# Kernel optimization log

Hardware: AMD Instinct MI355X
Metric: run time of the kernel (lower is better)

## Reference

```python
import jax, jax.numpy as jnp
import numpy as np

N_HEAD = 16
MA_K = 0.02          # sigmoid temperature in ma_k_activation
LEAKY_SLOPE = 0.02   # negative_slope in ma_q_activation
NEG_INF = -1e9


def setup_inputs() -> dict:
    key = jax.random.key(0)
    k1, k2, k3, k4 = jax.random.split(key, 4)
    B, T, C = 2, 2048, 1024
    x = jax.random.normal(k1, (B, T, C), dtype=jnp.float32)
    s = 1.0 / np.sqrt(C)
    W_attn = jax.random.normal(k2, (C, 2 * C), dtype=jnp.float32) * s
    W_k2 = jax.random.normal(k3, (C, C), dtype=jnp.float32) * s
    W_proj = jax.random.normal(k4, (C, C), dtype=jnp.float32) * s
    return {"x": x, "W_attn": W_attn, "W_k2": W_k2, "W_proj": W_proj}


def _heads(t, H):
    # [B,T,C] -> [B,H,T,d]
    B, T, C = t.shape
    return t.reshape(B, T, H, C // H).transpose(0, 2, 1, 3)


def reference(x, W_attn, W_k2, W_proj):
    B, T, C = x.shape
    H = N_HEAD
    d = C // H
    scale = 1.0 / jnp.sqrt(jnp.asarray(d, x.dtype))

    qk = x @ W_attn                      # [B,T,2C]
    q, k = jnp.split(qk, 2, axis=-1)
    q = _heads(q, H)                     # [B,H,T,d]
    k = _heads(k, H)
    v = _heads(x, H)                     # v = x

    # --- AR branch: causal softmax attention ---
    scores = jnp.einsum('bhtd,bhsd->bhts', q, k) * scale
    causal = jnp.tril(jnp.ones((T, T), dtype=bool))
    scores = jnp.where(causal, scores, NEG_INF)
    attn = jax.nn.softmax(scores, axis=-1)
    y = jnp.einsum('bhts,bhsd->bhtd', attn, v)   # [B,H,T,d]

    # --- MA branch: causal, softmax-free linear attention on residual ---
    e = v[:, :, 1:, :] - y[:, :, :-1, :]          # [B,H,T-1,d]
    k2 = _heads(x[:, :-1, :] @ W_k2, H)           # [B,H,T-1,d]
    q2 = q[:, :, 1:, :]                           # [B,H,T-1,d]

    qa = -jax.nn.leaky_relu(-q2 * scale, negative_slope=LEAKY_SLOPE)
    ka = jax.nn.sigmoid(MA_K * (k2 * scale))

    w = jnp.einsum('bhtd,bhsd->bhts', qa, ka)     # [B,H,T-1,T-1]
    w = jnp.tril(w)
    y2 = jnp.einsum('bhts,bhsd->bhtd', w, e)      # [B,H,T-1,d]
    y2 = jnp.concatenate([jnp.zeros_like(y2[:, :, :1, :]), y2], axis=2)  # pad front

    def merge(t):  # [B,H,T,d] -> [B,T,C]
        return t.transpose(0, 2, 1, 3).reshape(B, T, C)

    return merge(y) @ W_proj + merge(y2) @ W_proj
```

## Files before the change

kernel.cpp:

```cpp
#include <hip/hip_runtime.h>

typedef unsigned short u16;
typedef u16   u16x4  __attribute__((ext_vector_type(4)));
typedef u16   u16x8  __attribute__((ext_vector_type(8)));
typedef __bf16 bf16x8 __attribute__((ext_vector_type(8)));
typedef float  f32x4  __attribute__((ext_vector_type(4)));

__device__ __forceinline__ float bf2f(u16 v) {
    unsigned u = ((unsigned)v) << 16;
    return __builtin_bit_cast(float, u);
}
__device__ __forceinline__ u16 f2bf(float f) {
    unsigned u = __builtin_bit_cast(unsigned, f);
    u += 0x7fffu + ((u >> 16) & 1u);
    return (u16)(u >> 16);
}

__global__ __launch_bounds__(256)
void convert_f32_bf16(const float* __restrict__ in, u16* __restrict__ out, int n4) {
    int i = blockIdx.x * 256 + threadIdx.x;
    if (i < n4) {
        float4 v = ((const float4*)in)[i];
        u16x4 o;
        o.x = f2bf(v.x); o.y = f2bf(v.y); o.z = f2bf(v.z); o.w = f2bf(v.w);
        ((u16x4*)out)[i] = o;
    }
}

__global__ __launch_bounds__(256)
void transpose_f32_bf16(const float* __restrict__ in, u16* __restrict__ out,
                        int R, int Cd) {
    __shared__ u16 tile[64][65];
    const int c0 = blockIdx.x * 64, r0 = blockIdx.y * 64;
    const int tid = threadIdx.x;
#pragma unroll
    for (int i = 0; i < 16; ++i) {
        int idx = tid + i * 256;
        int r = idx >> 6, c = idx & 63;
        tile[r][c] = f2bf(in[(size_t)(r0 + r) * Cd + c0 + c]);
    }
    __syncthreads();
#pragma unroll
    for (int i = 0; i < 16; ++i) {
        int idx = tid + i * 256;
        int r = idx >> 6, c = idx & 63;
        out[(size_t)(c0 + r) * R + r0 + c] = tile[c][r];
    }
}

template <int EPI>
__global__ __launch_bounds__(256, 2)
void gemm_bt(const u16* __restrict__ A, const u16* __restrict__ Bt,
             void* __restrict__ Cv, int M, int N, int K) {
    __shared__ __align__(16) u16 As[4][128][8];
    __shared__ __align__(16) u16 Bs[4][128][8];
    const int tid = threadIdx.x;
    const int wave = tid >> 6, lane = tid & 63;
    const int m0 = blockIdx.y * 128, n0 = blockIdx.x * 128;
    const int wm = (wave >> 1) * 64, wn = (wave & 1) * 64;
    const int q = lane >> 4, mr = lane & 15;
    const int sr = tid >> 2, c8 = tid & 3;
    const u16* Ap = A + (size_t)(m0 + sr) * K + c8 * 8;
    const u16* Bp = Bt + (size_t)(n0 + sr) * K + c8 * 8;

    f32x4 acc[4][4];
#pragma unroll
    for (int i = 0; i < 4; ++i)
#pragma unroll
        for (int j = 0; j < 4; ++j) acc[i][j] = f32x4{0.f, 0.f, 0.f, 0.f};

    for (int k0 = 0; k0 < K; k0 += 32) {
        u16x8 a0 = *(const u16x8*)(Ap);
        u16x8 a1 = *(const u16x8*)(Ap + (size_t)64 * K);
        u16x8 b0 = *(const u16x8*)(Bp);
        u16x8 b1 = *(const u16x8*)(Bp + (size_t)64 * K);
        Ap += 32; Bp += 32;
        __syncthreads();
        *(u16x8*)&As[c8][sr][0]      = a0;
        *(u16x8*)&As[c8][sr + 64][0] = a1;
        *(u16x8*)&Bs[c8][sr][0]      = b0;
        *(u16x8*)&Bs[c8][sr + 64][0] = b1;
        __syncthreads();
        bf16x8 af[4], bfr[4];
#pragma unroll
        for (int i = 0; i < 4; ++i) af[i]  = *(const bf16x8*)&As[q][wm + i * 16 + mr][0];
#pragma unroll
        for (int j = 0; j < 4; ++j) bfr[j] = *(const bf16x8*)&Bs[q][wn + j * 16 + mr][0];
#pragma unroll
        for (int i = 0; i < 4; ++i)
#pragma unroll
            for (int j = 0; j < 4; ++j)
                acc[i][j] = __builtin_amdgcn_mfma_f32_16x16x32_bf16(af[i], bfr[j], acc[i][j], 0, 0, 0);
    }
    const float qsc = (n0 + wn < 1024) ? 0.125f : 1.0f;
#pragma unroll
    for (int i = 0; i < 4; ++i)
#pragma unroll
        for (int j = 0; j < 4; ++j)
#pragma unroll
            for (int r = 0; r < 4; ++r) {
                int m = m0 + wm + i * 16 + q * 4 + r;
                int n = n0 + wn + j * 16 + mr;
                float v = acc[i][j][r];
                if (EPI == 1)      ((float*)Cv)[(size_t)m * N + n] = v;
                else if (EPI == 2) ((u16*)Cv)[(size_t)m * N + n] = f2bf(1.f / (1.f + __expf(-0.0025f * v)));
                else               ((u16*)Cv)[(size_t)m * N + n] = f2bf(v * qsc);
            }
}

__global__ __launch_bounds__(256, 2)
void flash_mfma(const u16* __restrict__ qk, const u16* __restrict__ xb,
                const float* __restrict__ xf, u16* __restrict__ y,
                u16* __restrict__ eg) {
    __shared__ __align__(16) u16 Ks[8][64][8];
    __shared__ __align__(16) u16 Vs[8][64][8];
    __shared__ __align__(16) u16 Ps[4][16][72];
    const int bh = blockIdx.y, b = bh >> 4, h = bh & 15, hc = h * 64;
    const int tid = threadIdx.x, w = tid >> 6, lane = tid & 63;
    const int n16 = lane & 15, quad = lane >> 4;
    const int sK = tid >> 2, d0 = (tid & 3) * 8;
    const int vcol = lane;

    for (int rep = 0; rep < 2; ++rep) {
        const int tile = rep ? 31 - (int)blockIdx.x : (int)blockIdx.x;
        const int t0 = tile * 64;
        const int nchunk = tile + 1;

        bf16x8 qf[2];
        {
            const int trow = t0 + w * 16 + n16;
            const u16* qp = &qk[(size_t)(b * 2048 + trow) * 2048 + hc + quad * 8];
            qf[0] = *(const bf16x8*)qp;
            qf[1] = *(const bf16x8*)(qp + 32);
        }

        f32x4 O[4];
        float lsum[4];
#pragma unroll
        for (int jt = 0; jt < 4; ++jt) O[jt] = f32x4{0.f, 0.f, 0.f, 0.f};
#pragma unroll
        for (int r = 0; r < 4; ++r) lsum[r] = 0.f;

        u16x8 kr0, kr1;
        u16 vr[16];
        auto prefetch = [&](int s0) {
            size_t krow = (size_t)(b * 2048 + s0 + sK) * 2048 + 1024 + hc;
            kr0 = *(const u16x8*)&qk[krow + d0];
            kr1 = *(const u16x8*)&qk[krow + d0 + 32];
#pragma unroll
            for (int j = 0; j < 8; ++j) {
                vr[j]     = xb[(size_t)(b * 2048 + s0 + w * 8 + j) * 1024 + hc + vcol];
                vr[j + 8] = xb[(size_t)(b * 2048 + s0 + (w + 4) * 8 + j) * 1024 + hc + vcol];
            }
        };
        prefetch(0);

        for (int c = 0; c < nchunk; ++c) {
            const int s0 = c << 6;
            __syncthreads();
            *(u16x8*)&Ks[(d0 >> 3)][sK][0]     = kr0;
            *(u16x8*)&Ks[(d0 >> 3) + 4][sK][0] = kr1;
            {
                u16x8 va, vb;
#pragma unroll
                for (int j = 0; j < 8; ++j) { va[j] = vr[j]; vb[j] = vr[j + 8]; }
                *(u16x8*)&Vs[w][vcol][0]     = va;
                *(u16x8*)&Vs[w + 4][vcol][0] = vb;
            }
            __syncthreads();
            if (c + 1 < nchunk) prefetch(s0 + 64);

            f32x4 S[4];
#pragma unroll
            for (int jt = 0; jt < 4; ++jt) S[jt] = f32x4{0.f, 0.f, 0.f, 0.f};
#pragma unroll
            for (int ks = 0; ks < 2; ++ks)
#pragma unroll
                for (int jt = 0; jt < 4; ++jt) {
                    bf16x8 kf = *(const bf16x8*)&Ks[ks * 4 + quad][jt * 16 + n16][0];
                    S[jt] = __builtin_amdgcn_mfma_f32_16x16x32_bf16(qf[ks], kf, S[jt], 0, 0, 0);
                }

            float p[4][4];
#pragma unroll
            for (int reg = 0; reg < 4; ++reg)
#pragma unroll
                for (int jt = 0; jt < 4; ++jt)
                    p[reg][jt] = __expf(S[jt][reg] - 16.0f);
            if (c == nchunk - 1) {
#pragma unroll
                for (int reg = 0; reg < 4; ++reg) {
                    const int tr = t0 + w * 16 + quad * 4 + reg;
#pragma unroll
                    for (int jt = 0; jt < 4; ++jt)
                        if (s0 + jt * 16 + n16 > tr) p[reg][jt] = 0.f;
                }
            }
#pragma unroll
            for (int reg = 0; reg < 4; ++reg) {
                lsum[reg] += (p[reg][0] + p[reg][1]) + (p[reg][2] + p[reg][3]);
#pragma unroll
                for (int jt = 0; jt < 4; ++jt)
                    Ps[w][quad * 4 + reg][jt * 16 + n16] = f2bf(p[reg][jt]);
            }

            bf16x8 pf[2];
#pragma unroll
            for (int ks = 0; ks < 2; ++ks)
                pf[ks] = *(const bf16x8*)&Ps[w][n16][ks * 32 + quad * 8];
#pragma unroll
            for (int ks = 0; ks < 2; ++ks)
#pragma unroll
                for (int jt = 0; jt < 4; ++jt) {
                    bf16x8 vf = *(const bf16x8*)&Vs[ks * 4 + quad][jt * 16 + n16][0];
                    O[jt] = __builtin_amdgcn_mfma_f32_16x16x32_bf16(pf[ks], vf, O[jt], 0, 0, 0);
                }
        }

#pragma unroll
        for (int reg = 0; reg < 4; ++reg) {
            float l = lsum[reg];
#pragma unroll
            for (int off = 1; off < 16; off <<= 1) l += __shfl_xor(l, off, 64);
            const float inv = 1.f / l;
            const int tr = t0 + w * 16 + quad * 4 + reg;
            const size_t row = (size_t)(b * 2048 + tr) * 1024 + hc;
#pragma unroll
            for (int jt = 0; jt < 4; ++jt) {
                const int col = jt * 16 + n16;
                float yv = O[jt][reg] * inv;
                y[row + col] = f2bf(yv);
                float ev = (tr < 2047) ? xf[row + 1024 + col] - yv : 0.f;
                eg[row + col] = f2bf(ev);
            }
        }
    }
}

__global__ __launch_bounds__(256, 2)
void arma_mfma(const u16* __restrict__ qk, const u16* __restrict__ ka,
               const u16* __restrict__ eg, const u16* __restrict__ y,
               u16* __restrict__ ys) {
    __shared__ __align__(16) u16 Ks[8][64][8];
    __shared__ __align__(16) u16 Es[8][64][8];
    __shared__ __align__(16) u16 Ps[4][16][72];
    const int bh = blockIdx.y, b = bh >> 4, h = bh & 15, hc = h * 64;
    const int tid = threadIdx.x, w = tid >> 6, lane = tid & 63;
    const int n16 = lane & 15, quad = lane >> 4;
    const int sK = tid >> 2, d0 = (tid & 3) * 8;
    const int vcol = lane;

    for (int rep = 0; rep < 2; ++rep) {
        const int tile = rep ? 31 - (int)blockIdx.x : (int)blockIdx.x;
        const int t0 = tile * 64;
        const int nchunk = tile + 1;

        bf16x8 qf[2];
        {
            const int trow = t0 + w * 16 + n16;
            const u16* qp = &qk[(size_t)(b * 2048 + trow) * 2048 + hc + quad * 8];
#pragma unroll
            for (int ks = 0; ks < 2; ++ks) {
                u16x8 qv = *(const u16x8*)(qp + ks * 32);
                u16x8 o;
#pragma unroll
                for (int j = 0; j < 8; ++j) {
                    float z = bf2f(qv[j]);
                    o[j] = f2bf(z < 0.f ? z : 0.02f * z);
                }
                qf[ks] = __builtin_bit_cast(bf16x8, o);
            }
        }

        f32x4 O[4];
#pragma unroll
        for (int jt = 0; jt < 4; ++jt) O[jt] = f32x4{0.f, 0.f, 0.f, 0.f};

        u16x8 kr0, kr1;
        u16 vr[16];
        auto prefetch = [&](int s0) {
            size_t krow = (size_t)(b * 2048 + s0 + sK) * 1024 + hc;
            kr0 = *(const u16x8*)&ka[krow + d0];
            kr1 = *(const u16x8*)&ka[krow + d0 + 32];
#pragma unroll
            for (int j = 0; j < 8; ++j) {
                vr[j]     = eg[(size_t)(b * 2048 + s0 + w * 8 + j) * 1024 + hc + vcol];
                vr[j + 8] = eg[(size_t)(b * 2048 + s0 + (w + 4) * 8 + j) * 1024 + hc + vcol];
            }
        };
        prefetch(0);

        for (int c = 0; c < nchunk; ++c) {
            const int s0 = c << 6;
            __syncthreads();
            *(u16x8*)&Ks[(d0 >> 3)][sK][0]     = kr0;
            *(u16x8*)&Ks[(d0 >> 3) + 4][sK][0] = kr1;
            {
                u16x8 va, vb;
#pragma unroll
                for (int j = 0; j < 8; ++j) { va[j] = vr[j]; vb[j] = vr[j + 8]; }
                *(u16x8*)&Es[w][vcol][0]     = va;
                *(u16x8*)&Es[w + 4][vcol][0] = vb;
            }
            __syncthreads();
            if (c + 1 < nchunk) prefetch(s0 + 64);

            f32x4 S[4];
#pragma unroll
            for (int jt = 0; jt < 4; ++jt) S[jt] = f32x4{0.f, 0.f, 0.f, 0.f};
#pragma unroll
            for (int ks = 0; ks < 2; ++ks)
#pragma unroll
                for (int jt = 0; jt < 4; ++jt) {
                    bf16x8 kf = *(const bf16x8*)&Ks[ks * 4 + quad][jt * 16 + n16][0];
                    S[jt] = __builtin_amdgcn_mfma_f32_16x16x32_bf16(qf[ks], kf, S[jt], 0, 0, 0);
                }

            float p[4][4];
#pragma unroll
            for (int reg = 0; reg < 4; ++reg)
#pragma unroll
                for (int jt = 0; jt < 4; ++jt) p[reg][jt] = S[jt][reg];
            if (c == nchunk - 1) {
#pragma unroll
                for (int reg = 0; reg < 4; ++reg) {
                    const int tr = t0 + w * 16 + quad * 4 + reg;
#pragma unroll
                    for (int jt = 0; jt < 4; ++jt)
                        if (s0 + jt * 16 + n16 >= tr) p[reg][jt] = 0.f;
                }
            }
#pragma unroll
            for (int reg = 0; reg < 4; ++reg)
#pragma unroll
                for (int jt = 0; jt < 4; ++jt)
                    Ps[w][quad * 4 + reg][jt * 16 + n16] = f2bf(p[reg][jt]);

            bf16x8 pf[2];
#pragma unroll
            for (int ks = 0; ks < 2; ++ks)
                pf[ks] = *(const bf16x8*)&Ps[w][n16][ks * 32 + quad * 8];
#pragma unroll
            for (int ks = 0; ks < 2; ++ks)
#pragma unroll
                for (int jt = 0; jt < 4; ++jt) {
                    bf16x8 ef = *(const bf16x8*)&Es[ks * 4 + quad][jt * 16 + n16][0];
                    O[jt] = __builtin_amdgcn_mfma_f32_16x16x32_bf16(pf[ks], ef, O[jt], 0, 0, 0);
                }
        }

#pragma unroll
        for (int reg = 0; reg < 4; ++reg) {
            const int tr = t0 + w * 16 + quad * 4 + reg;
            const size_t row = (size_t)(b * 2048 + tr) * 1024 + hc;
#pragma unroll
            for (int jt = 0; jt < 4; ++jt) {
                const int col = jt * 16 + n16;
                ys[row + col] = f2bf(bf2f(y[row + col]) + O[jt][reg]);
            }
        }
    }
}

extern "C" void kernel_launch(void* const* d_in, const int* in_sizes, int n_in,
                              void* d_out, int out_size, void* d_ws, size_t ws_size,
                              hipStream_t stream) {
    const float* x      = (const float*)d_in[0];
    const float* W_attn = (const float*)d_in[1];
    const float* W_k2   = (const float*)d_in[2];
    const float* W_proj = (const float*)d_in[3];
    float* out = (float*)d_out;

    char* w = (char*)d_ws;
    u16* xb      = (u16*)w; w += (size_t)4096 * 1024 * 2;
    u16* Wt_attn = (u16*)w; w += (size_t)2048 * 1024 * 2;
    u16* Wt_k2   = (u16*)w; w += (size_t)1024 * 1024 * 2;
    u16* Wt_proj = (u16*)w; w += (size_t)1024 * 1024 * 2;
    u16* qk      = (u16*)w; w += (size_t)4096 * 2048 * 2;
    u16* ka      = (u16*)w; w += (size_t)4096 * 1024 * 2;
    u16* y       = (u16*)w; w += (size_t)4096 * 1024 * 2;
    u16* eg      = (u16*)w; w += (size_t)4096 * 1024 * 2;
    u16* ys      = (u16*)w; w += (size_t)4096 * 1024 * 2;

    convert_f32_bf16<<<dim3(4096), dim3(256), 0, stream>>>(x, xb, 1024 * 1024);
    transpose_f32_bf16<<<dim3(32, 16), dim3(256), 0, stream>>>(W_attn, Wt_attn, 1024, 2048);
    transpose_f32_bf16<<<dim3(16, 16), dim3(256), 0, stream>>>(W_k2,   Wt_k2,   1024, 1024);
    transpose_f32_bf16<<<dim3(16, 16), dim3(256), 0, stream>>>(W_proj, Wt_proj, 1024, 1024);
    gemm_bt<3><<<dim3(16, 32), dim3(256), 0, stream>>>(xb, Wt_attn, qk, 4096, 2048, 1024);
    gemm_bt<2><<<dim3(8, 32), dim3(256), 0, stream>>>(xb, Wt_k2, ka, 4096, 1024, 1024);
    flash_mfma<<<dim3(16, 32), dim3(256), 0, stream>>>(qk, xb, x, y, eg);
    arma_mfma<<<dim3(16, 32), dim3(256), 0, stream>>>(qk, ka, eg, y, ys);
    gemm_bt<1><<<dim3(8, 32), dim3(256), 0, stream>>>(ys, Wt_proj, out, 4096, 1024, 1024);
}
```

Baseline: 286.6 us.

## Pre-pack K/V tiles, split attention KV across two partitions, add combine kernels

K, sigmoid-K, V (x) and the residual e are now written by producer kernels in a pre-swizzled per-64-row tile layout, so the attention kernels load LDS tiles with contiguous 16-byte copies instead of strided scalar gathers. Both attention kernels split the key chunks between two z-partitions, raising occupancy (launch bounds 4). Separate combine kernels then sum the partials, normalise, and build y, e and ys. The GEMMs gain register prefetch of the next k-slice, and the N=1024 GEMMs use 64-row tiles for more blocks. This costs extra launches and extra global traffic for the bf16 partial outputs.

```diff
diff --git a/kernel.cpp b/kernel.cpp
--- a/kernel.cpp
+++ b/kernel.cpp
@@ -16,15 +16,29 @@
     return (u16)(u >> 16);
 }
 
+__device__ __forceinline__ size_t kimg_idx(int bh, int s, int d) {
+    return ((size_t)(bh * 32 + (s >> 6)) * 4096) + (size_t)(((d >> 3) * 64 + (s & 63)) * 8) + (d & 7);
+}
+__device__ __forceinline__ size_t vimg_idx(int bh, int s, int d) {
+    return ((size_t)(bh * 32 + (s >> 6)) * 4096) + (size_t)((((s & 63) >> 3) * 64 + d) * 8) + (s & 7);
+}
+
 __global__ __launch_bounds__(256)
-void convert_f32_bf16(const float* __restrict__ in, u16* __restrict__ out, int n4) {
+void convert_pack(const float* __restrict__ in, u16* __restrict__ xb,
+                  u16* __restrict__ xpack) {
     int i = blockIdx.x * 256 + threadIdx.x;
-    if (i < n4) {
-        float4 v = ((const float4*)in)[i];
-        u16x4 o;
-        o.x = f2bf(v.x); o.y = f2bf(v.y); o.z = f2bf(v.z); o.w = f2bf(v.w);
-        ((u16x4*)out)[i] = o;
-    }
+    int c4 = i & 255, row = i >> 8;
+    int s = row & 2047, b = row >> 11;
+    float4 v = ((const float4*)in)[i];
+    u16x4 o;
+    o.x = f2bf(v.x); o.y = f2bf(v.y); o.z = f2bf(v.z); o.w = f2bf(v.w);
+    ((u16x4*)xb)[i] = o;
+    int h = c4 >> 4, d0 = (c4 & 15) * 4;
+    size_t base = vimg_idx(b * 16 + h, s, d0);
+    xpack[base]      = o.x;
+    xpack[base + 8]  = o.y;
+    xpack[base + 16] = o.z;
+    xpack[base + 24] = o.w;
 }
 
 __global__ __launch_bounds__(256)
@@ -48,10 +62,9 @@
     }
 }
 
-template <int EPI>
 __global__ __launch_bounds__(256, 2)
-void gemm_bt(const u16* __restrict__ A, const u16* __restrict__ Bt,
-             void* __restrict__ Cv, int M, int N, int K) {
+void gemm_qk(const u16* __restrict__ A, const u16* __restrict__ Bt,
+             u16* __restrict__ qs, u16* __restrict__ kpack, int K) {
     __shared__ __align__(16) u16 As[4][128][8];
     __shared__ __align__(16) u16 Bs[4][128][8];
     const int tid = threadIdx.x;
@@ -69,18 +82,22 @@
 #pragma unroll
         for (int j = 0; j < 4; ++j) acc[i][j] = f32x4{0.f, 0.f, 0.f, 0.f};
 
+    u16x8 a0, a1, b0, b1;
+    auto gload = [&](int k0) {
+        a0 = *(const u16x8*)(Ap + k0);
+        a1 = *(const u16x8*)(Ap + k0 + (size_t)64 * K);
+        b0 = *(const u16x8*)(Bp + k0);
+        b1 = *(const u16x8*)(Bp + k0 + (size_t)64 * K);
+    };
+    gload(0);
     for (int k0 = 0; k0 < K; k0 += 32) {
-        u16x8 a0 = *(const u16x8*)(Ap);
-        u16x8 a1 = *(const u16x8*)(Ap + (size_t)64 * K);
-        u16x8 b0 = *(const u16x8*)(Bp);
-        u16x8 b1 = *(const u16x8*)(Bp + (size_t)64 * K);
-        Ap += 32; Bp += 32;
         __syncthreads();
         *(u16x8*)&As[c8][sr][0]      = a0;
         *(u16x8*)&As[c8][sr + 64][0] = a1;
         *(u16x8*)&Bs[c8][sr][0]      = b0;
         *(u16x8*)&Bs[c8][sr + 64][0] = b1;
         __syncthreads();
+        if (k0 + 32 < K) gload(k0 + 32);
         bf16x8 af[4], bfr[4];
 #pragma unroll
         for (int i = 0; i < 4; ++i) af[i]  = *(const bf16x8*)&As[q][wm + i * 16 + mr][0];
@@ -92,7 +109,6 @@
             for (int j = 0; j < 4; ++j)
                 acc[i][j] = __builtin_amdgcn_mfma_f32_16x16x32_bf16(af[i], bfr[j], acc[i][j], 0, 0, 0);
     }
-    const float qsc = (n0 + wn < 1024) ? 0.125f : 1.0f;
 #pragma unroll
     for (int i = 0; i < 4; ++i)
 #pragma unroll
@@ -102,24 +118,95 @@
                 int m = m0 + wm + i * 16 + q * 4 + r;
                 int n = n0 + wn + j * 16 + mr;
                 float v = acc[i][j][r];
-                if (EPI == 1)      ((float*)Cv)[(size_t)m * N + n] = v;
-                else if (EPI == 2) ((u16*)Cv)[(size_t)m * N + n] = f2bf(1.f / (1.f + __expf(-0.0025f * v)));
-                else               ((u16*)Cv)[(size_t)m * N + n] = f2bf(v * qsc);
+                if (n < 1024) {
+                    qs[(size_t)m * 1024 + n] = f2bf(v * 0.125f);
+                } else {
+                    int b = m >> 11, s = m & 2047, nn = n - 1024;
+                    kpack[kimg_idx(b * 16 + (nn >> 6), s, nn & 63)] = f2bf(v);
+                }
             }
 }
 
+template <int EPI>
 __global__ __launch_bounds__(256, 2)
-void flash_mfma(const u16* __restrict__ qk, const u16* __restrict__ xb,
-                const float* __restrict__ xf, u16* __restrict__ y,
-                u16* __restrict__ eg) {
+void gemm64(const u16* __restrict__ A, const u16* __restrict__ Bt,
+            void* __restrict__ Cv, int N, int K) {
+    __shared__ __align__(16) u16 As[4][64][8];
+    __shared__ __align__(16) u16 Bs[4][128][8];
+    const int tid = threadIdx.x;
+    const int wave = tid >> 6, lane = tid & 63;
+    const int m0 = blockIdx.y * 64, n0 = blockIdx.x * 128;
+    const int wn0 = wave * 32;
+    const int q = lane >> 4, mr = lane & 15;
+    const int sr = tid >> 2, c8 = tid & 3;
+    const u16* Ap = A + (size_t)(m0 + sr) * K + c8 * 8;
+    const u16* Bp = Bt + (size_t)(n0 + sr) * K + c8 * 8;
+
+    f32x4 acc[4][2];
+#pragma unroll
+    for (int i = 0; i < 4; ++i)
+#pragma unroll
+        for (int j = 0; j < 2; ++j) acc[i][j] = f32x4{0.f, 0.f, 0.f, 0.f};
+
+    u16x8 a0, b0, b1;
+    auto gload = [&](int k0) {
+        a0 = *(const u16x8*)(Ap + k0);
+        b0 = *(const u16x8*)(Bp + k0);
+        b1 = *(const u16x8*)(Bp + k0 + (size_t)64 * K);
+    };
+    gload(0);
+    for (int k0 = 0; k0 < K; k0 += 32) {
+        __syncthreads();
+        *(u16x8*)&As[c8][sr][0]      = a0;
+        *(u16x8*)&Bs[c8][sr][0]      = b0;
+        *(u16x8*)&Bs[c8][sr + 64][0] = b1;
+        __syncthreads();
+        if (k0 + 32 < K) gload(k0 + 32);
+        bf16x8 af[4], bfr[2];
+#pragma unroll
+        for (int i = 0; i < 4; ++i) af[i]  = *(const bf16x8*)&As[q][i * 16 + mr][0];
+#pragma unroll
+        for (int j = 0; j < 2; ++j) bfr[j] = *(const bf16x8*)&Bs[q][wn0 + j * 16 + mr][0];
+#pragma unroll
+        for (int i = 0; i < 4; ++i)
+#pragma unroll
+            for (int j = 0; j < 2; ++j)
+                acc[i][j] = __builtin_amdgcn_mfma_f32_16x16x32_bf16(af[i], bfr[j], acc[i][j], 0, 0, 0);
+    }
+#pragma unroll
+    for (int i = 0; i < 4; ++i)
+#pragma unroll
+        for (int j = 0; j < 2; ++j)
+#pragma unroll
+            for (int r = 0; r < 4; ++r) {
+                int m = m0 + i * 16 + q * 4 + r;
+                int n = n0 + wn0 + j * 16 + mr;
+                float v = acc[i][j][r];
+                if (EPI == 1) {
+                    ((float*)Cv)[(size_t)m * N + n] = v;
+                } else {
+                    int b = m >> 11, s = m & 2047;
+                    ((u16*)Cv)[kimg_idx(b * 16 + (n >> 6), s, n & 63)] =
+                        f2bf(1.f / (1.f + __expf(-0.0025f * v)));
+                }
+            }
+}
+
+__global__ __launch_bounds__(256, 4)
+void flash_mfma(const u16* __restrict__ qs, const u16* __restrict__ kpack,
+                const u16* __restrict__ xpack, u16* __restrict__ Opart,
+                float* __restrict__ lpart) {
     __shared__ __align__(16) u16 Ks[8][64][8];
     __shared__ __align__(16) u16 Vs[8][64][8];
     __shared__ __align__(16) u16 Ps[4][16][72];
-    const int bh = blockIdx.y, b = bh >> 4, h = bh & 15, hc = h * 64;
+    const int bh = blockIdx.y, b = bh >> 4, hc = (bh & 15) * 64;
+    const int z = blockIdx.z;
     const int tid = threadIdx.x, w = tid >> 6, lane = tid & 63;
     const int n16 = lane & 15, quad = lane >> 4;
-    const int sK = tid >> 2, d0 = (tid & 3) * 8;
-    const int vcol = lane;
+    const u16* kbase = kpack + (size_t)bh * 32 * 4096;
+    const u16* vbase = xpack + (size_t)bh * 32 * 4096;
+    u16* Ob = Opart + (size_t)z * 4096 * 1024;
+    float* lb = lpart + z * 65536;
 
     for (int rep = 0; rep < 2; ++rep) {
         const int tile = rep ? 31 - (int)blockIdx.x : (int)blockIdx.x;
@@ -129,7 +216,7 @@
         bf16x8 qf[2];
         {
             const int trow = t0 + w * 16 + n16;
-            const u16* qp = &qk[(size_t)(b * 2048 + trow) * 2048 + hc + quad * 8];
+            const u16* qp = &qs[(size_t)(b * 2048 + trow) * 1024 + hc + quad * 8];
             qf[0] = *(const bf16x8*)qp;
             qf[1] = *(const bf16x8*)(qp + 32);
         }
@@ -141,34 +228,25 @@
 #pragma unroll
         for (int r = 0; r < 4; ++r) lsum[r] = 0.f;
 
-        u16x8 kr0, kr1;
-        u16 vr[16];
-        auto prefetch = [&](int s0) {
-            size_t krow = (size_t)(b * 2048 + s0 + sK) * 2048 + 1024 + hc;
-            kr0 = *(const u16x8*)&qk[krow + d0];
-            kr1 = *(const u16x8*)&qk[krow + d0 + 32];
-#pragma unroll
-            for (int j = 0; j < 8; ++j) {
-                vr[j]     = xb[(size_t)(b * 2048 + s0 + w * 8 + j) * 1024 + hc + vcol];
-                vr[j + 8] = xb[(size_t)(b * 2048 + s0 + (w + 4) * 8 + j) * 1024 + hc + vcol];
-            }
+        u16x8 kr0, kr1, vr0, vr1;
+        auto pref = [&](int c) {
+            const u16* kc = kbase + (size_t)c * 4096;
+            const u16* vc = vbase + (size_t)c * 4096;
+            kr0 = *(const u16x8*)(kc + tid * 8);
+            kr1 = *(const u16x8*)(kc + (256 + tid) * 8);
+            vr0 = *(const u16x8*)(vc + tid * 8);
+            vr1 = *(const u16x8*)(vc + (256 + tid) * 8);
         };
-        prefetch(0);
-
-        for (int c = 0; c < nchunk; ++c) {
-            const int s0 = c << 6;
+        if (z < nchunk) pref(z);
+
+        for (int c = z; c < nchunk; c += 2) {
             __syncthreads();
-            *(u16x8*)&Ks[(d0 >> 3)][sK][0]     = kr0;
-            *(u16x8*)&Ks[(d0 >> 3) + 4][sK][0] = kr1;
-            {
-                u16x8 va, vb;
-#pragma unroll
-                for (int j = 0; j < 8; ++j) { va[j] = vr[j]; vb[j] = vr[j + 8]; }
-                *(u16x8*)&Vs[w][vcol][0]     = va;
-                *(u16x8*)&Vs[w + 4][vcol][0] = vb;
-            }
+            *(u16x8*)((u16*)Ks + tid * 8)         = kr0;
+            *(u16x8*)((u16*)Ks + (256 + tid) * 8) = kr1;
+            *(u16x8*)((u16*)Vs + tid * 8)         = vr0;
+            *(u16x8*)((u16*)Vs + (256 + tid) * 8) = vr1;
             __syncthreads();
-            if (c + 1 < nchunk) prefetch(s0 + 64);
+            if (c + 2 < nchunk) pref(c + 2);
 
             f32x4 S[4];
 #pragma unroll
@@ -187,13 +265,13 @@
 #pragma unroll
                 for (int jt = 0; jt < 4; ++jt)
                     p[reg][jt] = __expf(S[jt][reg] - 16.0f);
-            if (c == nchunk - 1) {
+            if (c == tile) {
 #pragma unroll
                 for (int reg = 0; reg < 4; ++reg) {
-                    const int tr = t0 + w * 16 + quad * 4 + reg;
+                    const int tr = w * 16 + quad * 4 + reg;
 #pragma unroll
                     for (int jt = 0; jt < 4; ++jt)
-                        if (s0 + jt * 16 + n16 > tr) p[reg][jt] = 0.f;
+                        if (jt * 16 + n16 > tr) p[reg][jt] = 0.f;
                 }
             }
 #pragma unroll
@@ -222,33 +300,61 @@
             float l = lsum[reg];
 #pragma unroll
             for (int off = 1; off < 16; off <<= 1) l += __shfl_xor(l, off, 64);
-            const float inv = 1.f / l;
             const int tr = t0 + w * 16 + quad * 4 + reg;
+            if (n16 == 0) lb[bh * 2048 + tr] = l;
             const size_t row = (size_t)(b * 2048 + tr) * 1024 + hc;
 #pragma unroll
-            for (int jt = 0; jt < 4; ++jt) {
-                const int col = jt * 16 + n16;
-                float yv = O[jt][reg] * inv;
-                y[row + col] = f2bf(yv);
-                float ev = (tr < 2047) ? xf[row + 1024 + col] - yv : 0.f;
-                eg[row + col] = f2bf(ev);
-            }
+            for (int jt = 0; jt < 4; ++jt)
+                Ob[row + jt * 16 + n16] = f2bf(O[jt][reg]);
         }
     }
 }
 
-__global__ __launch_bounds__(256, 2)
-void arma_mfma(const u16* __restrict__ qk, const u16* __restrict__ ka,
-               const u16* __restrict__ eg, const u16* __restrict__ y,
-               u16* __restrict__ ys) {
+__global__ __launch_bounds__(256)
+void combine_flash(const u16* __restrict__ Opart, const float* __restrict__ lpart,
+                   const u16* __restrict__ xb, u16* __restrict__ y,
+                   u16* __restrict__ epack) {
+    int i = blockIdx.x * 256 + threadIdx.x;
+    int c4 = i & 255, row = i >> 8, t = row & 2047, b = row >> 11;
+    int h = c4 >> 4, d0 = (c4 & 15) * 4;
+    size_t off = (size_t)row * 1024 + c4 * 4;
+    u16x4 o0 = *(const u16x4*)&Opart[off];
+    u16x4 o1 = *(const u16x4*)&Opart[(size_t)4096 * 1024 + off];
+    int lrow = (b * 16 + h) * 2048 + t;
+    float inv = 1.f / (lpart[lrow] + lpart[65536 + lrow]);
+    float y0 = (bf2f(o0.x) + bf2f(o1.x)) * inv;
+    float y1 = (bf2f(o0.y) + bf2f(o1.y)) * inv;
+    float y2 = (bf2f(o0.z) + bf2f(o1.z)) * inv;
+    float y3 = (bf2f(o0.w) + bf2f(o1.w)) * inv;
+    u16x4 yo;
+    yo.x = f2bf(y0); yo.y = f2bf(y1); yo.z = f2bf(y2); yo.w = f2bf(y3);
+    *(u16x4*)&y[off] = yo;
+    float e0 = 0.f, e1 = 0.f, e2 = 0.f, e3 = 0.f;
+    if (t < 2047) {
+        u16x4 xv = *(const u16x4*)&xb[off + 1024];
+        e0 = bf2f(xv.x) - y0; e1 = bf2f(xv.y) - y1;
+        e2 = bf2f(xv.z) - y2; e3 = bf2f(xv.w) - y3;
+    }
+    size_t base = vimg_idx(b * 16 + h, t, d0);
+    epack[base]      = f2bf(e0);
+    epack[base + 8]  = f2bf(e1);
+    epack[base + 16] = f2bf(e2);
+    epack[base + 24] = f2bf(e3);
+}
+
+__global__ __launch_bounds__(256, 4)
+void arma_mfma(const u16* __restrict__ qs, const u16* __restrict__ kapack,
+               const u16* __restrict__ epack, u16* __restrict__ Opart) {
     __shared__ __align__(16) u16 Ks[8][64][8];
     __shared__ __align__(16) u16 Es[8][64][8];
     __shared__ __align__(16) u16 Ps[4][16][72];
-    const int bh = blockIdx.y, b = bh >> 4, h = bh & 15, hc = h * 64;
+    const int bh = blockIdx.y, b = bh >> 4, hc = (bh & 15) * 64;
+    const int z = blockIdx.z;
     const int tid = threadIdx.x, w = tid >> 6, lane = tid & 63;
     const int n16 = lane & 15, quad = lane >> 4;
-    const int sK = tid >> 2, d0 = (tid & 3) * 8;
-    const int vcol = lane;
+    const u16* kbase = kapack + (size_t)bh * 32 * 4096;
+    const u16* vbase = epack + (size_t)bh * 32 * 4096;
+    u16* Ob = Opart + (size_t)z * 4096 * 1024;
 
     for (int rep = 0; rep < 2; ++rep) {
         const int tile = rep ? 31 - (int)blockIdx.x : (int)blockIdx.x;
@@ -258,15 +364,15 @@
         bf16x8 qf[2];
         {
             const int trow = t0 + w * 16 + n16;
-            const u16* qp = &qk[(size_t)(b * 2048 + trow) * 2048 + hc + quad * 8];
+            const u16* qp = &qs[(size_t)(b * 2048 + trow) * 1024 + hc + quad * 8];
 #pragma unroll
             for (int ks = 0; ks < 2; ++ks) {
                 u16x8 qv = *(const u16x8*)(qp + ks * 32);
                 u16x8 o;
 #pragma unroll
                 for (int j = 0; j < 8; ++j) {
-                    float z = bf2f(qv[j]);
-                    o[j] = f2bf(z < 0.f ? z : 0.02f * z);
+                    float zv = bf2f(qv[j]);
+                    o[j] = f2bf(zv < 0.f ? zv : 0.02f * zv);
                 }
                 qf[ks] = __builtin_bit_cast(bf16x8, o);
             }
@@ -276,34 +382,25 @@
 #pragma unroll
         for (int jt = 0; jt < 4; ++jt) O[jt] = f32x4{0.f, 0.f, 0.f, 0.f};
 
-        u16x8 kr0, kr1;
-        u16 vr[16];
-        auto prefetch = [&](int s0) {
-            size_t krow = (size_t)(b * 2048 + s0 + sK) * 1024 + hc;
-            kr0 = *(const u16x8*)&ka[krow + d0];
-            kr1 = *(const u16x8*)&ka[krow + d0 + 32];
-#pragma unroll
-            for (int j = 0; j < 8; ++j) {
-                vr[j]     = eg[(size_t)(b * 2048 + s0 + w * 8 + j) * 1024 + hc + vcol];
-                vr[j + 8] = eg[(size_t)(b * 2048 + s0 + (w + 4) * 8 + j) * 1024 + hc + vcol];
-            }
+        u16x8 kr0, kr1, vr0, vr1;
+        auto pref = [&](int c) {
+            const u16* kc = kbase + (size_t)c * 4096;
+            const u16* vc = vbase + (size_t)c * 4096;
+            kr0 = *(const u16x8*)(kc + tid * 8);
+            kr1 = *(const u16x8*)(kc + (256 + tid) * 8);
+            vr0 = *(const u16x8*)(vc + tid * 8);
+            vr1 = *(const u16x8*)(vc + (256 + tid) * 8);
         };
-        prefetch(0);
-
-        for (int c = 0; c < nchunk; ++c) {
-            const int s0 = c << 6;
+        if (z < nchunk) pref(z);
+
+        for (int c = z; c < nchunk; c += 2) {
             __syncthreads();
-            *(u16x8*)&Ks[(d0 >> 3)][sK][0]     = kr0;
-            *(u16x8*)&Ks[(d0 >> 3) + 4][sK][0] = kr1;
-            {
-                u16x8 va, vb;
-#pragma unroll
-                for (int j = 0; j < 8; ++j) { va[j] = vr[j]; vb[j] = vr[j + 8]; }
-                *(u16x8*)&Es[w][vcol][0]     = va;
-                *(u16x8*)&Es[w + 4][vcol][0] = vb;
-            }
+            *(u16x8*)((u16*)Ks + tid * 8)         = kr0;
+            *(u16x8*)((u16*)Ks + (256 + tid) * 8) = kr1;
+            *(u16x8*)((u16*)Es + tid * 8)         = vr0;
+            *(u16x8*)((u16*)Es + (256 + tid) * 8) = vr1;
             __syncthreads();
-            if (c + 1 < nchunk) prefetch(s0 + 64);
+            if (c + 2 < nchunk) pref(c + 2);
 
             f32x4 S[4];
 #pragma unroll
@@ -316,25 +413,20 @@
                     S[jt] = __builtin_amdgcn_mfma_f32_16x16x32_bf16(qf[ks], kf, S[jt], 0, 0, 0);
                 }
 
-            float p[4][4];
+            if (c == tile) {
+#pragma unroll
+                for (int reg = 0; reg < 4; ++reg) {
+                    const int tr = w * 16 + quad * 4 + reg;
+#pragma unroll
+                    for (int jt = 0; jt < 4; ++jt)
+                        if (jt * 16 + n16 >= tr) S[jt][reg] = 0.f;
+                }
+            }
 #pragma unroll
             for (int reg = 0; reg < 4; ++reg)
 #pragma unroll
-                for (int jt = 0; jt < 4; ++jt) p[reg][jt] = S[jt][reg];
-            if (c == nchunk - 1) {
-#pragma unroll
-                for (int reg = 0; reg < 4; ++reg) {
-                    const int tr = t0 + w * 16 + quad * 4 + reg;
-#pragma unroll
-                    for (int jt = 0; jt < 4; ++jt)
-                        if (s0 + jt * 16 + n16 >= tr) p[reg][jt] = 0.f;
-                }
-            }
-#pragma unroll
-            for (int reg = 0; reg < 4; ++reg)
-#pragma unroll
                 for (int jt = 0; jt < 4; ++jt)
-                    Ps[w][quad * 4 + reg][jt * 16 + n16] = f2bf(p[reg][jt]);
+                    Ps[w][quad * 4 + reg][jt * 16 + n16] = f2bf(S[jt][reg]);
 
             bf16x8 pf[2];
 #pragma unroll
@@ -354,12 +446,26 @@
             const int tr = t0 + w * 16 + quad * 4 + reg;
             const size_t row = (size_t)(b * 2048 + tr) * 1024 + hc;
 #pragma unroll
-            for (int jt = 0; jt < 4; ++jt) {
-                const int col = jt * 16 + n16;
-                ys[row + col] = f2bf(bf2f(y[row + col]) + O[jt][reg]);
-            }
+            for (int jt = 0; jt < 4; ++jt)
+                Ob[row + jt * 16 + n16] = f2bf(O[jt][reg]);
         }
     }
+}
+
+__global__ __launch_bounds__(256)
+void combine_arma(const u16* __restrict__ Opart, const u16* __restrict__ y,
+                  u16* __restrict__ ys) {
+    int i = blockIdx.x * 256 + threadIdx.x;
+    size_t off = (size_t)i * 4;
+    u16x4 o0 = *(const u16x4*)&Opart[off];
+    u16x4 o1 = *(const u16x4*)&Opart[(size_t)4096 * 1024 + off];
+    u16x4 yv = *(const u16x4*)&y[off];
+    u16x4 r;
+    r.x = f2bf(bf2f(yv.x) + bf2f(o0.x) + bf2f(o1.x));
+    r.y = f2bf(bf2f(yv.y) + bf2f(o0.y) + bf2f(o1.y));
+    r.z = f2bf(bf2f(yv.z) + bf2f(o0.z) + bf2f(o1.z));
+    r.w = f2bf(bf2f(yv.w) + bf2f(o0.w) + bf2f(o1.w));
+    *(u16x4*)&ys[off] = r;
 }
 
 extern "C" void kernel_launch(void* const* d_in, const int* in_sizes, int n_in,
@@ -376,19 +482,25 @@
     u16* Wt_attn = (u16*)w; w += (size_t)2048 * 1024 * 2;
     u16* Wt_k2   = (u16*)w; w += (size_t)1024 * 1024 * 2;
     u16* Wt_proj = (u16*)w; w += (size_t)1024 * 1024 * 2;
-    u16* qk      = (u16*)w; w += (size_t)4096 * 2048 * 2;
-    u16* ka      = (u16*)w; w += (size_t)4096 * 1024 * 2;
+    u16* qs      = (u16*)w; w += (size_t)4096 * 1024 * 2;
+    u16* kpack   = (u16*)w; w += (size_t)4096 * 1024 * 2;
+    u16* kapack  = (u16*)w; w += (size_t)4096 * 1024 * 2;
+    u16* xpack   = (u16*)w; w += (size_t)4096 * 1024 * 2;
     u16* y       = (u16*)w; w += (size_t)4096 * 1024 * 2;
-    u16* eg      = (u16*)w; w += (size_t)4096 * 1024 * 2;
-    u16* ys      = (u16*)w; w += (size_t)4096 * 1024 * 2;
-
-    convert_f32_bf16<<<dim3(4096), dim3(256), 0, stream>>>(x, xb, 1024 * 1024);
+    u16* epack   = (u16*)w; w += (size_t)4096 * 1024 * 2;
+    u16* Opart   = (u16*)w; w += (size_t)2 * 4096 * 1024 * 2;
+    float* lpart = (float*)w; w += (size_t)2 * 65536 * 4;
+    u16* ys = xb;
+
+    convert_pack<<<dim3(4096), dim3(256), 0, stream>>>(x, xb, xpack);
     transpose_f32_bf16<<<dim3(32, 16), dim3(256), 0, stream>>>(W_attn, Wt_attn, 1024, 2048);
     transpose_f32_bf16<<<dim3(16, 16), dim3(256), 0, stream>>>(W_k2,   Wt_k2,   1024, 1024);
     transpose_f32_bf16<<<dim3(16, 16), dim3(256), 0, stream>>>(W_proj, Wt_proj, 1024, 1024);
-    gemm_bt<3><<<dim3(16, 32), dim3(256), 0, stream>>>(xb, Wt_attn, qk, 4096, 2048, 1024);
-    gemm_bt<2><<<dim3(8, 32), dim3(256), 0, stream>>>(xb, Wt_k2, ka, 4096, 1024, 1024);
-    flash_mfma<<<dim3(16, 32), dim3(256), 0, stream>>>(qk, xb, x, y, eg);
-    arma_mfma<<<dim3(16, 32), dim3(256), 0, stream>>>(qk, ka, eg, y, ys);
-    gemm_bt<1><<<dim3(8, 32), dim3(256), 0, stream>>>(ys, Wt_proj, out, 4096, 1024, 1024);
-}
+    gemm_qk<<<dim3(16, 32), dim3(256), 0, stream>>>(xb, Wt_attn, qs, kpack, 1024);
+    gemm64<2><<<dim3(8, 64), dim3(256), 0, stream>>>(xb, Wt_k2, kapack, 1024, 1024);
+    flash_mfma<<<dim3(16, 32, 2), dim3(256), 0, stream>>>(qs, kpack, xpack, Opart, lpart);
+    combine_flash<<<dim3(4096), dim3(256), 0, stream>>>(Opart, lpart, xb, y, epack);
+    arma_mfma<<<dim3(16, 32, 2), dim3(256), 0, stream>>>(qs, kapack, epack, Opart);
+    combine_arma<<<dim3(4096), dim3(256), 0, stream>>>(Opart, y, ys);
+    gemm64<1><<<dim3(8, 64), dim3(256), 0, stream>>>(ys, Wt_proj, out, 1024, 1024);
+}
```

Measured after the change: 307.8 us. 1.07x slower.
